# Performance work log

Hardware: AMD Instinct MI355X
Metric: run time of the kernel (lower is better)

The kernel has to match this reference:

```python
import jax, jax.numpy as jnp
import numpy as np

NUM_LAYERS = 5
EMB_DIM = 300
NUM_ATOM_TYPE = 121
NUM_CHIRALITY = 11
NUM_BOND_TYPE = 7
NUM_BOND_DIR = 3
BN_EPS = 1e-5


def setup_inputs() -> dict:
    key = jax.random.key(0)
    ks = jax.random.split(key, 16)
    N, E, D, L = 100000, 200000, EMB_DIM, NUM_LAYERS

    def glorot(k, shape):
        fan_in, fan_out = shape[-2], shape[-1]
        s = jnp.sqrt(6.0 / (fan_in + fan_out))
        return jax.random.uniform(k, shape, jnp.float32, -s, s)

    x = jax.random.randint(ks[0], (N, 2), 0, 11)  # atom type / chirality (both < 11, in range)
    edge_index = jax.random.randint(ks[1], (2, E), 0, N)
    edge_attr = jax.random.randint(ks[2], (E, 2), 0, 3)

    return {
        "x": x,
        "edge_index": edge_index,
        "edge_attr": edge_attr,
        "x_emb1": glorot(ks[3], (NUM_ATOM_TYPE, D)),
        "x_emb2": glorot(ks[4], (NUM_CHIRALITY, D)),
        "edge_emb1": glorot(ks[5], (L, NUM_BOND_TYPE, D)),
        "edge_emb2": glorot(ks[6], (L, NUM_BOND_DIR, D)),
        "w1": glorot(ks[7], (L, D, 2 * D)),
        "b1": jnp.zeros((L, 2 * D), jnp.float32),
        "w2": glorot(ks[8], (L, 2 * D, D)),
        "b2": jnp.zeros((L, D), jnp.float32),
        "bn_gamma": jnp.ones((L, D), jnp.float32),
        "bn_beta": jnp.zeros((L, D), jnp.float32),
    }


def reference(x, edge_index, edge_attr, x_emb1, x_emb2, edge_emb1, edge_emb2,
              w1, b1, w2, b2, bn_gamma, bn_beta):
    N = x.shape[0]
    # GINConv.forward adds self loops with edge_attr row [4, 0]
    loop = jnp.arange(N)
    src = jnp.concatenate([edge_index[0], loop])  # [E+N]
    dst = jnp.concatenate([edge_index[1], loop])  # [E+N]
    ea0 = jnp.concatenate([edge_attr[:, 0], jnp.full((N,), 4, edge_attr.dtype)])
    ea1 = jnp.concatenate([edge_attr[:, 1], jnp.zeros((N,), edge_attr.dtype)])

    # node input embedding
    h = x_emb1[x[:, 0]] + x_emb2[x[:, 1]]  # [N, D]

    for l in range(NUM_LAYERS):
        # edge embeddings (incl. self loops)
        eemb = edge_emb1[l][ea0] + edge_emb2[l][ea1]  # [E+N, D]
        # message: x_j + edge_attr, aggr='add' at destination nodes
        msg = h[src] + eemb
        agg = jax.ops.segment_sum(msg, dst, num_segments=N)  # [N, D]
        # GIN update MLP: Linear(D, 2D) -> ReLU -> Linear(2D, D)
        h2 = jax.nn.relu(agg @ w1[l] + b1[l]) @ w2[l] + b2[l]
        # BatchNorm1d (training mode: batch statistics, biased variance)
        mean = h2.mean(axis=0)
        var = h2.var(axis=0)
        h2 = (h2 - mean) * jax.lax.rsqrt(var + BN_EPS) * bn_gamma[l] + bn_beta[l]
        # ReLU on all but last layer (dropout is identity, drop_ratio=0)
        if l < NUM_LAYERS - 1:
            h2 = jax.nn.relu(h2)
        h = h2
    # JK == 'last'
    return h
```

## Files before the change

kernel.cpp:

```cpp
#include <hip/hip_runtime.h>
#include <hip/hip_bf16.h>
#include <stdint.h>

typedef __bf16 bf16_t;
typedef bf16_t bf16x8 __attribute__((ext_vector_type(8)));
typedef float  f32x4  __attribute__((ext_vector_type(4)));

__device__ __forceinline__ void g2l16(const void* gp, void* lp) {
  __builtin_amdgcn_global_load_lds(
      (const __attribute__((address_space(1))) unsigned int*)(uintptr_t)gp,
      (__attribute__((address_space(3))) unsigned int*)(uint32_t)(uintptr_t)lp,
      16, 0, 0);
}

__global__ void embed_kernel(const int* __restrict__ x, const float* __restrict__ e1,
                             const float* __restrict__ e2, bf16_t* __restrict__ h, int N) {
  const int w = (blockIdx.x * blockDim.x + threadIdx.x) >> 6;
  const int lane = threadIdx.x & 63;
  if (w >= N || lane >= 40) return;
  const int t0 = x[2 * w], t1 = x[2 * w + 1];
  const int co = lane * 8;
  f32x4 a0 = *(const f32x4*)&e1[t0 * 300 + co];
  f32x4 a1 = *(const f32x4*)&e1[t0 * 300 + co + 4];
  f32x4 b0 = *(const f32x4*)&e2[t1 * 300 + co];
  f32x4 b1 = *(const f32x4*)&e2[t1 * 300 + co + 4];
  bf16x8 o;
  #pragma unroll
  for (int j = 0; j < 8; j++) {
    float v = (j < 4) ? (a0[j] + b0[j]) : (a1[j - 4] + b1[j - 4]);
    o[j] = (co + j < 300) ? (bf16_t)v : (bf16_t)0.f;
  }
  *(bf16x8*)&h[(size_t)w * 320 + co] = o;
}

__global__ void count_deg_kernel(const int* __restrict__ ei, int* __restrict__ deg, int E) {
  int e = blockIdx.x * 256 + threadIdx.x;
  if (e < E) atomicAdd(&deg[ei[E + e]], 1);
}

__global__ void scan_partial_kernel(const int* __restrict__ deg, int* __restrict__ part, int N) {
  __shared__ int s[256];
  const int tid = threadIdx.x;
  const int idx = blockIdx.x * 256 + tid;
  s[tid] = (idx < N) ? deg[idx] : 0;
  __syncthreads();
  for (int off = 128; off > 0; off >>= 1) {
    if (tid < off) s[tid] += s[tid + off];
    __syncthreads();
  }
  if (tid == 0) part[blockIdx.x] = s[0];
}

__global__ void scan_block_kernel(int* __restrict__ part, int n) {
  __shared__ int s[1024];
  const int tid = threadIdx.x;
  const int v = (tid < n) ? part[tid] : 0;
  s[tid] = v;
  __syncthreads();
  for (int off = 1; off < 1024; off <<= 1) {
    int x = (tid >= off) ? s[tid - off] : 0;
    __syncthreads();
    s[tid] += x;
    __syncthreads();
  }
  if (tid < n) part[tid] = s[tid] - v;
}

__global__ void scan_final_kernel(const int* __restrict__ deg, const int* __restrict__ part,
                                  int* __restrict__ rowptr, int* __restrict__ cursor, int N, int E) {
  __shared__ int s[256];
  const int tid = threadIdx.x;
  const int idx = blockIdx.x * 256 + tid;
  const int v = (idx < N) ? deg[idx] : 0;
  s[tid] = v;
  __syncthreads();
  for (int off = 1; off < 256; off <<= 1) {
    int x = (tid >= off) ? s[tid - off] : 0;
    __syncthreads();
    s[tid] += x;
    __syncthreads();
  }
  if (idx < N) {
    int ex = s[tid] - v + part[blockIdx.x];
    rowptr[idx] = ex;
    cursor[idx] = ex;
  }
  if (idx == 0) rowptr[N] = E;
}

__global__ void fill_csr_kernel(const int* __restrict__ ei, const int* __restrict__ ea,
                                int* __restrict__ cursor, int* __restrict__ epack, int E) {
  int e = blockIdx.x * 256 + threadIdx.x;
  if (e >= E) return;
  int slot = atomicAdd(&cursor[ei[E + e]], 1);
  int a = ea[2 * e] * 3 + ea[2 * e + 1];
  epack[slot] = (ei[e] & 0xFFFFF) | (a << 20);
}

__global__ void convert_w1_kernel(const float* __restrict__ w1, bf16_t* __restrict__ o) {
  int id = blockIdx.x * 256 + threadIdx.x;
  if (id >= 5 * 640 * 320) return;
  int k = id % 320;
  int n = (id / 320) % 640;
  int l = id / (320 * 640);
  float v = (k < 300 && n < 600) ? w1[(size_t)l * 300 * 600 + (size_t)k * 600 + n] : 0.f;
  o[id] = (bf16_t)v;
}

__global__ void convert_w2_kernel(const float* __restrict__ w2, bf16_t* __restrict__ o) {
  int id = blockIdx.x * 256 + threadIdx.x;
  if (id >= 5 * 384 * 640) return;
  int k = id % 640;
  int n = (id / 640) % 384;
  int l = id / (640 * 384);
  float v = (k < 600 && n < 300) ? w2[(size_t)l * 600 * 300 + (size_t)k * 300 + n] : 0.f;
  o[id] = (bf16_t)v;
}

__global__ void build_t12_kernel(const float* __restrict__ ee1, const float* __restrict__ ee2,
                                 bf16_t* __restrict__ T12) {
  int id = blockIdx.x * 256 + threadIdx.x;
  if (id >= 5 * 21 * 320) return;
  int col = id % 320;
  int r = id / 320;
  int l = r / 21;
  int a = r % 21;
  int a0 = a / 3, a1 = a % 3;
  float v = 0.f;
  if (col < 300) v = ee1[((size_t)l * 7 + a0) * 300 + col] + ee2[((size_t)l * 3 + a1) * 300 + col];
  T12[id] = (bf16_t)v;
}

template <bool FUSE_BN>
__global__ void aggregate_kernel(const bf16_t* __restrict__ hsrc, const int* __restrict__ rowptr,
                                 const int* __restrict__ epack, const bf16_t* __restrict__ T12L,
                                 const float* __restrict__ scale, const float* __restrict__ shift,
                                 bf16_t* __restrict__ agg, int N, int LDH) {
  const int g = blockIdx.x * 256 + threadIdx.x;
  const int w = g / 40;
  if (w >= N) return;
  const int co = (g - w * 40) * 8;

  float sc[8], sh[8];
  if (FUSE_BN) {
    f32x4 s0 = *(const f32x4*)&scale[co];
    f32x4 s1 = *(const f32x4*)&scale[co + 4];
    f32x4 t0 = *(const f32x4*)&shift[co];
    f32x4 t1 = *(const f32x4*)&shift[co + 4];
    #pragma unroll
    for (int j = 0; j < 4; j++) { sc[j] = s0[j]; sc[j + 4] = s1[j]; sh[j] = t0[j]; sh[j + 4] = t1[j]; }
  }

  const int beg = rowptr[w], end = rowptr[w + 1];
  float acc[8];
  {
    bf16x8 hv = *(const bf16x8*)&hsrc[(size_t)w * LDH + co];
    bf16x8 tv = *(const bf16x8*)&T12L[12 * 320 + co];
    #pragma unroll
    for (int j = 0; j < 8; j++) {
      float v = (float)hv[j];
      if (FUSE_BN) v = fmaxf(v * sc[j] + sh[j], 0.f);
      acc[j] = v + (float)tv[j];
    }
  }
  for (int e = beg; e < end; e++) {
    const int p = epack[e];
    const int s = p & 0xFFFFF;
    const int a = (p >> 20) & 0x1F;
    bf16x8 hv = *(const bf16x8*)&hsrc[(size_t)s * LDH + co];
    bf16x8 tv = *(const bf16x8*)&T12L[a * 320 + co];
    #pragma unroll
    for (int j = 0; j < 8; j++) {
      float v = (float)hv[j];
      if (FUSE_BN) v = fmaxf(v * sc[j] + sh[j], 0.f);
      acc[j] += v + (float)tv[j];
    }
  }
  bf16x8 o;
  #pragma unroll
  for (int j = 0; j < 8; j++) o[j] = (bf16_t)acc[j];
  *(bf16x8*)&agg[(size_t)w * 320 + co] = o;
}

template <int LDA, int LDB, int LDC, int NK, int GY, int NBIAS, bool RELU, bool STATS>
__global__ __launch_bounds__(256) void gemm_kernel(const bf16_t* __restrict__ A,
                                                   const bf16_t* __restrict__ BT,
                                                   const float* __restrict__ bias,
                                                   bf16_t* __restrict__ C,
                                                   float* __restrict__ sums,
                                                   float* __restrict__ sumsq,
                                                   int Nvalid, int nwg) {
  __shared__ __align__(16) bf16_t As0[128 * 32];
  __shared__ __align__(16) bf16_t Bs0[128 * 32];
  __shared__ __align__(16) bf16_t As1[128 * 32];
  __shared__ __align__(16) bf16_t Bs1[128 * 32];
  __shared__ __align__(16) bf16_t As2[128 * 32];
  __shared__ __align__(16) bf16_t Bs2[128 * 32];

  const int tid = threadIdx.x;
  const int lane = tid & 63;
  const int wave = tid >> 6;
  const int ml = lane & 15, quad = lane >> 4;
  const int wm = (wave & 1) * 64, wn = (wave >> 1) * 64;
  const int kx = (ml >> 1) & 3;

  const int bid = blockIdx.x;
  const int q = nwg >> 3, r = nwg & 7;
  const int xcd = bid & 7, pos = bid >> 3;
  const int logical = (xcd < r ? xcd * (q + 1) : r * (q + 1) + (xcd - r) * q) + pos;
  const size_t bm = (size_t)(logical / GY) * 128;
  const size_t bnn = (size_t)(logical % GY) * 128;

  const int srow = tid >> 2;
  const int cg = (tid & 3) ^ ((tid >> 3) & 3);
  const bf16_t* ag = A + (bm + srow) * LDA + cg * 8;
  const bf16_t* bg = BT + (bnn + srow) * LDB + cg * 8;

  auto stage = [&](bf16_t* as, bf16_t* bs, int kb) {
    const int kof = kb * 32;
    #pragma unroll
    for (int it = 0; it < 2; it++) {
      g2l16(ag + (size_t)it * 64 * LDA + kof, (void*)&as[((size_t)it * 256 + tid) * 8]);
      g2l16(bg + (size_t)it * 64 * LDB + kof, (void*)&bs[((size_t)it * 256 + tid) * 8]);
    }
  };
  auto bufA = [&](int i) -> bf16_t* { return i == 0 ? As0 : (i == 1 ? As1 : As2); };
  auto bufB = [&](int i) -> bf16_t* { return i == 0 ? Bs0 : (i == 1 ? Bs1 : Bs2); };

  f32x4 acc[4][4];
  #pragma unroll
  for (int rr = 0; rr < 4; rr++)
    #pragma unroll
    for (int cc = 0; cc < 4; cc++) acc[rr][cc] = (f32x4){0.f, 0.f, 0.f, 0.f};

  auto compute = [&](const bf16_t* as, const bf16_t* bs) {
    const int ck = quad ^ kx;
    bf16x8 aF[4], bF[4];
    #pragma unroll
    for (int mf = 0; mf < 4; mf++)
      aF[mf] = *(const bf16x8*)&as[((wm + mf * 16 + ml) * 4 + ck) * 8];
    #pragma unroll
    for (int nf = 0; nf < 4; nf++)
      bF[nf] = *(const bf16x8*)&bs[((wn + nf * 16 + ml) * 4 + ck) * 8];
    #pragma unroll
    for (int mf = 0; mf < 4; mf++)
      #pragma unroll
      for (int nf = 0; nf < 4; nf++)
        acc[mf][nf] = __builtin_amdgcn_mfma_f32_16x16x32_bf16(aF[mf], bF[nf], acc[mf][nf], 0, 0, 0);
  };

  stage(As0, Bs0, 0);
  stage(As1, Bs1, 1);

  #pragma unroll
  for (int kb = 0; kb < NK; kb++) {
    if (kb + 2 < NK) {
      stage(bufA((kb + 2) % 3), bufB((kb + 2) % 3), kb + 2);
      asm volatile("s_waitcnt vmcnt(8)" ::: "memory");
    } else if (kb + 1 < NK) {
      asm volatile("s_waitcnt vmcnt(4)" ::: "memory");
    } else {
      asm volatile("s_waitcnt vmcnt(0)" ::: "memory");
    }
    __builtin_amdgcn_s_barrier();
    __builtin_amdgcn_sched_barrier(0);
    compute(bufA(kb % 3), bufB(kb % 3));
    __builtin_amdgcn_sched_barrier(0);
    __builtin_amdgcn_s_barrier();
  }

  #pragma unroll
  for (int nf = 0; nf < 4; nf++) {
    const int colg = (int)bnn + wn + nf * 16 + ml;
    const float bv = (colg < NBIAS) ? bias[colg] : 0.f;
    float s = 0.f, sq = 0.f;
    #pragma unroll
    for (int mf = 0; mf < 4; mf++) {
      #pragma unroll
      for (int i = 0; i < 4; i++) {
        const size_t rowg = bm + wm + mf * 16 + quad * 4 + i;
        float v = acc[mf][nf][i] + bv;
        if (RELU) v = fmaxf(v, 0.f);
        C[rowg * LDC + colg] = (bf16_t)v;
        if (STATS) {
          const bool ok = rowg < (size_t)Nvalid;
          s += ok ? v : 0.f;
          sq += ok ? v * v : 0.f;
        }
      }
    }
    if (STATS) {
      s += __shfl_down(s, 16);
      sq += __shfl_down(sq, 16);
      s += __shfl_down(s, 32);
      sq += __shfl_down(sq, 32);
      if (quad == 0) {
        atomicAdd(&sums[colg], s);
        atomicAdd(&sumsq[colg], sq);
      }
    }
  }
}

__global__ void bn_params_kernel(const float* __restrict__ sums, const float* __restrict__ sumsq,
                                 const float* __restrict__ gamma, const float* __restrict__ beta,
                                 float* __restrict__ scale, float* __restrict__ shift, int N) {
  const int col = threadIdx.x;
  if (col >= 384) return;
  if (col >= 300) {
    scale[col] = 0.f;
    shift[col] = 0.f;
    return;
  }
  const float inv = 1.f / (float)N;
  const float mean = sums[col] * inv;
  float var = sumsq[col] * inv - mean * mean;
  if (var < 0.f) var = 0.f;
  const float sc = gamma[col] * rsqrtf(var + 1e-5f);
  scale[col] = sc;
  shift[col] = beta[col] - mean * sc;
}

__global__ void bn_apply_kernel(const bf16_t* __restrict__ H2, const float* __restrict__ scale,
                                const float* __restrict__ shift, float* __restrict__ out, int N) {
  const int w = (blockIdx.x * blockDim.x + threadIdx.x) >> 6;
  const int lane = threadIdx.x & 63;
  if (w >= N || lane >= 40) return;
  const int co = lane * 8;
  bf16x8 v8 = *(const bf16x8*)&H2[(size_t)w * 384 + co];
  f32x4 s0 = *(const f32x4*)&scale[co];
  f32x4 s1 = *(const f32x4*)&scale[co + 4];
  f32x4 t0 = *(const f32x4*)&shift[co];
  f32x4 t1 = *(const f32x4*)&shift[co + 4];
  #pragma unroll
  for (int j = 0; j < 8; j++) {
    float sc = (j < 4) ? s0[j] : s1[j - 4];
    float sh = (j < 4) ? t0[j] : t1[j - 4];
    float v = (float)v8[j] * sc + sh;
    if (co + j < 300) out[(size_t)w * 300 + co + j] = v;
  }
}

extern "C" void kernel_launch(void* const* d_in, const int* in_sizes, int n_in,
                              void* d_out, int out_size, void* d_ws, size_t ws_size,
                              hipStream_t stream) {
  const int* x = (const int*)d_in[0];
  const int* ei = (const int*)d_in[1];
  const int* ea = (const int*)d_in[2];
  const float* xe1 = (const float*)d_in[3];
  const float* xe2 = (const float*)d_in[4];
  const float* ee1 = (const float*)d_in[5];
  const float* ee2 = (const float*)d_in[6];
  const float* w1 = (const float*)d_in[7];
  const float* b1 = (const float*)d_in[8];
  const float* w2 = (const float*)d_in[9];
  const float* b2 = (const float*)d_in[10];
  const float* gam = (const float*)d_in[11];
  const float* bet = (const float*)d_in[12];

  const int N = in_sizes[0] / 2;
  const int E = in_sizes[1] / 2;
  const int Mt = (N + 127) / 128;
  const size_t Mp = (size_t)Mt * 128;

  char* p = (char*)d_ws;
  auto take = [&](size_t b) -> char* {
    char* r = p;
    p += (b + 255) & ~(size_t)255;
    return r;
  };
  bf16_t* h    = (bf16_t*)take(Mp * 320 * 2);
  bf16_t* agg  = (bf16_t*)take(Mp * 320 * 2);
  bf16_t* C1   = (bf16_t*)take(Mp * 640 * 2);
  bf16_t* H2   = (bf16_t*)take(Mp * 384 * 2);
  bf16_t* W1bT = (bf16_t*)take((size_t)5 * 640 * 320 * 2);
  bf16_t* W2bT = (bf16_t*)take((size_t)5 * 384 * 640 * 2);
  bf16_t* T12  = (bf16_t*)take((size_t)5 * 21 * 320 * 2);
  int* deg     = (int*)take((size_t)N * 4);
  int* rowptr  = (int*)take((size_t)(N + 1) * 4);
  int* cursor  = (int*)take((size_t)N * 4);
  int* part    = (int*)take(1024 * 4);
  int* epack   = (int*)take((size_t)E * 4);
  float* sums  = (float*)take(384 * 4);
  float* sumsq = (float*)take(384 * 4);
  float* scale = (float*)take(384 * 4);
  float* shift = (float*)take(384 * 4);

  hipMemsetAsync(agg, 0, Mp * 320 * 2, stream);
  hipMemsetAsync(deg, 0, (size_t)N * 4, stream);

  const int nwb = (N + 3) / 4;
  embed_kernel<<<nwb, 256, 0, stream>>>(x, xe1, xe2, h, N);

  count_deg_kernel<<<(E + 255) / 256, 256, 0, stream>>>(ei, deg, E);
  const int nsb = (N + 255) / 256;
  scan_partial_kernel<<<nsb, 256, 0, stream>>>(deg, part, N);
  scan_block_kernel<<<1, 1024, 0, stream>>>(part, nsb);
  scan_final_kernel<<<nsb, 256, 0, stream>>>(deg, part, rowptr, cursor, N, E);
  fill_csr_kernel<<<(E + 255) / 256, 256, 0, stream>>>(ei, ea, cursor, epack, E);

  convert_w1_kernel<<<(5 * 640 * 320 + 255) / 256, 256, 0, stream>>>(w1, W1bT);
  convert_w2_kernel<<<(5 * 384 * 640 + 255) / 256, 256, 0, stream>>>(w2, W2bT);
  build_t12_kernel<<<(5 * 21 * 320 + 255) / 256, 256, 0, stream>>>(ee1, ee2, T12);

  const int nwg1 = Mt * 5;
  const int nwg2 = Mt * 3;
  const int nab = (N * 40 + 255) / 256;

  for (int l = 0; l < 5; l++) {
    if (l == 0) {
      aggregate_kernel<false><<<nab, 256, 0, stream>>>(h, rowptr, epack,
                                                       T12 + (size_t)l * 21 * 320,
                                                       scale, shift, agg, N, 320);
    } else {
      aggregate_kernel<true><<<nab, 256, 0, stream>>>(H2, rowptr, epack,
                                                      T12 + (size_t)l * 21 * 320,
                                                      scale, shift, agg, N, 384);
    }
    gemm_kernel<320, 320, 640, 10, 5, 600, true, false>
        <<<nwg1, 256, 0, stream>>>(agg, W1bT + (size_t)l * 640 * 320,
                                   b1 + (size_t)l * 600, C1, sums, sumsq, N, nwg1);
    hipMemsetAsync(sums, 0, 384 * 4, stream);
    hipMemsetAsync(sumsq, 0, 384 * 4, stream);
    gemm_kernel<640, 640, 384, 20, 3, 300, false, true>
        <<<nwg2, 256, 0, stream>>>(C1, W2bT + (size_t)l * 384 * 640,
                                   b2 + (size_t)l * 300, H2, sums, sumsq, N, nwg2);
    bn_params_kernel<<<1, 384, 0, stream>>>(sums, sumsq, gam + (size_t)l * 300,
                                            bet + (size_t)l * 300, scale, shift, N);
  }
  bn_apply_kernel<<<nwb, 256, 0, stream>>>(H2, scale, shift, (float*)d_out, N);
}
```

Measured before the change: 1.367 ms.

## Replace direct-to-LDS triple buffering with register-staged double buffering in GEMM

The GEMM mainloop no longer uses global_load_lds into three LDS stages. It now loads A tiles two steps ahead and B tiles one step ahead into registers, then writes them into two LDS buffers after each compute step, with one barrier per iteration. LDS use drops from three stages to two and launch bounds request 3 blocks per CU, aiming for higher occupancy and fewer barriers. In exchange it needs extra VGPRs and explicit LDS stores, and with only one k-step of lookahead it may hide less memory latency.

```diff
diff --git a/kernel.cpp b/kernel.cpp
--- a/kernel.cpp
+++ b/kernel.cpp
@@ -5,13 +5,6 @@
 typedef __bf16 bf16_t;
 typedef bf16_t bf16x8 __attribute__((ext_vector_type(8)));
 typedef float  f32x4  __attribute__((ext_vector_type(4)));
-
-__device__ __forceinline__ void g2l16(const void* gp, void* lp) {
-  __builtin_amdgcn_global_load_lds(
-      (const __attribute__((address_space(1))) unsigned int*)(uintptr_t)gp,
-      (__attribute__((address_space(3))) unsigned int*)(uint32_t)(uintptr_t)lp,
-      16, 0, 0);
-}
 
 __global__ void embed_kernel(const int* __restrict__ x, const float* __restrict__ e1,
                              const float* __restrict__ e2, bf16_t* __restrict__ h, int N) {
@@ -183,19 +176,17 @@
 }
 
 template <int LDA, int LDB, int LDC, int NK, int GY, int NBIAS, bool RELU, bool STATS>
-__global__ __launch_bounds__(256) void gemm_kernel(const bf16_t* __restrict__ A,
-                                                   const bf16_t* __restrict__ BT,
-                                                   const float* __restrict__ bias,
-                                                   bf16_t* __restrict__ C,
-                                                   float* __restrict__ sums,
-                                                   float* __restrict__ sumsq,
-                                                   int Nvalid, int nwg) {
+__global__ __launch_bounds__(256, 3) void gemm_kernel(const bf16_t* __restrict__ A,
+                                                      const bf16_t* __restrict__ BT,
+                                                      const float* __restrict__ bias,
+                                                      bf16_t* __restrict__ C,
+                                                      float* __restrict__ sums,
+                                                      float* __restrict__ sumsq,
+                                                      int Nvalid, int nwg) {
   __shared__ __align__(16) bf16_t As0[128 * 32];
   __shared__ __align__(16) bf16_t Bs0[128 * 32];
   __shared__ __align__(16) bf16_t As1[128 * 32];
   __shared__ __align__(16) bf16_t Bs1[128 * 32];
-  __shared__ __align__(16) bf16_t As2[128 * 32];
-  __shared__ __align__(16) bf16_t Bs2[128 * 32];
 
   const int tid = threadIdx.x;
   const int lane = tid & 63;
@@ -216,16 +207,23 @@
   const bf16_t* ag = A + (bm + srow) * LDA + cg * 8;
   const bf16_t* bg = BT + (bnn + srow) * LDB + cg * 8;
 
-  auto stage = [&](bf16_t* as, bf16_t* bs, int kb) {
+  auto loadA = [&](int kb, bf16x8& r0, bf16x8& r1) {
     const int kof = kb * 32;
-    #pragma unroll
-    for (int it = 0; it < 2; it++) {
-      g2l16(ag + (size_t)it * 64 * LDA + kof, (void*)&as[((size_t)it * 256 + tid) * 8]);
-      g2l16(bg + (size_t)it * 64 * LDB + kof, (void*)&bs[((size_t)it * 256 + tid) * 8]);
-    }
+    r0 = *(const bf16x8*)(ag + kof);
+    r1 = *(const bf16x8*)(ag + (size_t)64 * LDA + kof);
   };
-  auto bufA = [&](int i) -> bf16_t* { return i == 0 ? As0 : (i == 1 ? As1 : As2); };
-  auto bufB = [&](int i) -> bf16_t* { return i == 0 ? Bs0 : (i == 1 ? Bs1 : Bs2); };
+  auto loadB = [&](int kb, bf16x8& r0, bf16x8& r1) {
+    const int kof = kb * 32;
+    r0 = *(const bf16x8*)(bg + kof);
+    r1 = *(const bf16x8*)(bg + (size_t)64 * LDB + kof);
+  };
+  auto store = [&](bf16_t* as, bf16_t* bs, const bf16x8& a0, const bf16x8& a1,
+                   const bf16x8& b0, const bf16x8& b1) {
+    *(bf16x8*)&as[(size_t)tid * 8] = a0;
+    *(bf16x8*)&as[(256 + (size_t)tid) * 8] = a1;
+    *(bf16x8*)&bs[(size_t)tid * 8] = b0;
+    *(bf16x8*)&bs[(256 + (size_t)tid) * 8] = b1;
+  };
 
   f32x4 acc[4][4];
   #pragma unroll
@@ -249,24 +247,27 @@
         acc[mf][nf] = __builtin_amdgcn_mfma_f32_16x16x32_bf16(aF[mf], bF[nf], acc[mf][nf], 0, 0, 0);
   };
 
-  stage(As0, Bs0, 0);
-  stage(As1, Bs1, 1);
+  bf16x8 a[2][2], b[2];
+  loadA(0, a[0][0], a[0][1]);
+  loadB(0, b[0], b[1]);
+  loadA(1, a[1][0], a[1][1]);
+  store(As0, Bs0, a[0][0], a[0][1], b[0], b[1]);
+  asm volatile("s_waitcnt lgkmcnt(0)" ::: "memory");
+  __builtin_amdgcn_s_barrier();
+  __builtin_amdgcn_sched_barrier(0);
 
   #pragma unroll
   for (int kb = 0; kb < NK; kb++) {
-    if (kb + 2 < NK) {
-      stage(bufA((kb + 2) % 3), bufB((kb + 2) % 3), kb + 2);
-      asm volatile("s_waitcnt vmcnt(8)" ::: "memory");
-    } else if (kb + 1 < NK) {
-      asm volatile("s_waitcnt vmcnt(4)" ::: "memory");
-    } else {
-      asm volatile("s_waitcnt vmcnt(0)" ::: "memory");
-    }
-    __builtin_amdgcn_s_barrier();
-    __builtin_amdgcn_sched_barrier(0);
-    compute(bufA(kb % 3), bufB(kb % 3));
-    __builtin_amdgcn_sched_barrier(0);
-    __builtin_amdgcn_s_barrier();
+    if (kb + 1 < NK) loadB(kb + 1, b[0], b[1]);
+    if (kb + 2 < NK) loadA(kb + 2, a[kb % 2][0], a[kb % 2][1]);
+    if ((kb & 1) == 0) compute(As0, Bs0); else compute(As1, Bs1);
+    if (kb + 1 < NK) {
+      if ((kb & 1) == 0) store(As1, Bs1, a[(kb + 1) % 2][0], a[(kb + 1) % 2][1], b[0], b[1]);
+      else               store(As0, Bs0, a[(kb + 1) % 2][0], a[(kb + 1) % 2][1], b[0], b[1]);
+      asm volatile("s_waitcnt lgkmcnt(0)" ::: "memory");
+      __builtin_amdgcn_s_barrier();
+      __builtin_amdgcn_sched_barrier(0);
+    }
   }
 
   #pragma unroll
```

Measured after the change: 1.367 ms. About the same (-0.0%).
